# Optimization experiments

Measured on AMD Instinct MI355X. Metric: run time of the kernel, lower is better.

Reference implementation:

```python
import jax, jax.numpy as jnp
import numpy as np

S = 16        # neighbor samples per layer
NL = 2        # number of GNN layers


def setup_inputs() -> dict:
    key = jax.random.key(0)
    ks = jax.random.split(key, 12)
    N_NODES, D, E, NMP, DEG, N_EDGE, B, NC = 50000, 128, 32, 3, 32, 200000, 1024, 8
    sc = 0.05
    return {
        "ids": jax.random.randint(ks[0], (B,), 0, N_NODES, dtype=jnp.int32),
        "feats": jax.random.normal(ks[1], (N_NODES, D), jnp.float32),
        "edge_emb": jax.random.normal(ks[2], (NMP, N_EDGE, E), jnp.float32),
        "adj_nodes": jax.random.randint(ks[3], (NMP, N_NODES, DEG), 0, N_NODES, dtype=jnp.int32),
        "adj_edges": jax.random.randint(ks[4], (NMP, N_NODES, DEG), 0, N_EDGE, dtype=jnp.int32),
        "W_self": jax.random.normal(ks[5], (NMP, NL, D, D), jnp.float32) * sc,
        "W_neigh": jax.random.normal(ks[6], (NMP, NL, D + E, D), jnp.float32) * sc,
        "W_edge": jax.random.normal(ks[7], (NMP, NL, 2 * D + E, E), jnp.float32) * sc,
        "attn": jax.random.normal(ks[8], (D,), jnp.float32) * sc,
        "fc_w": jax.random.normal(ks[9], (D, NC), jnp.float32) * sc,
        "fc_b": jnp.zeros((NC,), jnp.float32),
    }


def reference(ids, feats, edge_emb, adj_nodes, adj_edges, W_self, W_neigh, W_edge, attn, fc_w, fc_b):
    NMP = adj_nodes.shape[0]
    outs = []
    for mp in range(NMP):
        # --- sample neighbor tree (deterministic: first S columns) ---
        cur = ids
        all_feats = [feats[cur]]
        all_edges = []
        for _ in range(NL):
            nb = adj_nodes[mp][cur][:, :S].reshape(-1)     # [N*S]
            eid = adj_edges[mp][cur][:, :S].reshape(-1)    # [N*S]
            all_edges.append(edge_emb[mp][eid])            # [N*S, E]
            cur = nb
            all_feats.append(feats[cur])
        # --- per-layer aggregation + edge update ---
        for l in range(NL):
            new_feats = []
            for k in range(len(all_feats) - 1):
                xs, xn, ee = all_feats[k], all_feats[k + 1], all_edges[k]
                N = xs.shape[0]
                # mean over sampled neighbors of [neigh_feat || edge_emb]
                nin = jnp.concatenate(
                    [xn.reshape(N, S, -1), ee.reshape(N, S, -1)], axis=-1
                ).mean(axis=1)                             # [N, D+E]
                new_feats.append(jax.nn.relu(xs @ W_self[mp, l] + nin @ W_neigh[mp, l]))
            all_feats = new_feats  # dropout is identity in eval mode
            new_edges = []
            for k in range(len(all_edges) - 1):
                xs, xn, ee = all_feats[k], all_feats[k + 1], all_edges[k]
                rep = jnp.repeat(xs, S, axis=0)            # [N*S, D]
                new_edges.append(jax.nn.relu(
                    jnp.concatenate([rep, xn, ee], axis=-1) @ W_edge[mp, l]))
            all_edges = new_edges
        outs.append(all_feats[0])                          # [B, D]
    stacked = jnp.stack(outs)                              # [NMP, B, D]
    # metapath attention fuse
    scores = jnp.tanh(jnp.einsum('mbd,d->mb', stacked, attn))
    beta = jax.nn.softmax(scores, axis=0)
    emb = jnp.einsum('mb,mbd->bd', beta, stacked)          # [B, D]
    # F.normalize(dim=1)
    emb = emb / jnp.maximum(jnp.linalg.norm(emb, axis=1, keepdims=True), 1e-12)
    return emb @ fc_w + fc_b
```

## Files before the change

kernel.cpp:

```cpp
#include <hip/hip_runtime.h>

#define NNODES  50000
#define D       128
#define E       32
#define NMP     3
#define DEG     32
#define NEDGE   200000
#define B       1024
#define NC      8
#define S       16

#define RPM      17408
#define NKT      9
#define WSTRIDE  36864
#define WESTRIDE 9216

#define CONV_TASKS (1600000 + 6 * WSTRIDE + 3 * WESTRIDE)
#define TOT_TASKS  (CONV_TASKS + 3 * RPM)

typedef float f4 __attribute__((ext_vector_type(4)));
typedef short bh8 __attribute__((ext_vector_type(8)));

static __device__ __forceinline__ unsigned short f2bf(float f) {
    unsigned int u = __float_as_uint(f);
    u = u + 0x7FFFu + ((u >> 16) & 1u);
    return (unsigned short)(u >> 16);
}
static __device__ __forceinline__ float bf2f(unsigned short h) {
    return __uint_as_float(((unsigned int)h) << 16);
}

__global__ __launch_bounds__(256) void convsamp_k(
    const float* __restrict__ feats, const float* __restrict__ Ws,
    const float* __restrict__ Wn, const float* __restrict__ We,
    const int* __restrict__ ids, const int* __restrict__ adjn,
    const int* __restrict__ adje,
    unsigned short* __restrict__ fb, unsigned short* __restrict__ WT0,
    unsigned short* __restrict__ WTe, int* __restrict__ gx, int* __restrict__ eid1)
{
    int i = blockIdx.x * 256 + threadIdx.x;
    if (i < 1600000) {
        float4 v = ((const float4*)feats)[i];
        unsigned int p0 = (unsigned int)f2bf(v.x) | ((unsigned int)f2bf(v.y) << 16);
        unsigned int p1 = (unsigned int)f2bf(v.z) | ((unsigned int)f2bf(v.w) << 16);
        ((uint2*)fb)[i] = make_uint2(p0, p1);
    } else if (i < 1600000 + 6 * WSTRIDE) {
        int i2 = i - 1600000;
        int ml = i2 / WSTRIDE, e = i2 % WSTRIDE;
        int j = e & 7, t1 = e >> 3;
        int n = t1 & 127, t2 = t1 >> 7;
        int q = t2 & 3, kt = t2 >> 2;
        int k = kt * 32 + q * 8 + j;
        float v = (k < 128) ? Ws[((size_t)ml * 128 + k) * 128 + n]
                            : Wn[((size_t)ml * 160 + (k - 128)) * 128 + n];
        WT0[(size_t)ml * WSTRIDE + e] = f2bf(v);
    } else if (i < CONV_TASKS) {
        int i3 = i - 1600000 - 6 * WSTRIDE;
        int mp = i3 / WESTRIDE, e = i3 % WESTRIDE;
        int j = e & 7, t1 = e >> 3;
        int n = t1 & 31, t2 = t1 >> 5;
        int q = t2 & 3, kt = t2 >> 2;
        int k = kt * 32 + q * 8 + j;
        float v = We[(((size_t)mp * 2) * 288 + k) * 32 + n];
        WTe[(size_t)mp * WESTRIDE + e] = f2bf(v);
    } else if (i < TOT_TASKS) {
        int i4 = i - CONV_TASKS;
        int mp = i4 / RPM, r = i4 % RPM;
        if (r < 16384) {
            int node = ids[r >> 4];
            gx[mp * RPM + r]   = adjn[((size_t)mp * NNODES + node) * DEG + (r & 15)];
            eid1[mp * 16384 + r] = adje[((size_t)mp * NNODES + node) * DEG + (r & 15)];
        } else {
            gx[mp * RPM + r] = ids[r - 16384];
        }
    }
}

__global__ __launch_bounds__(256) void aggnin_k(
    const unsigned short* __restrict__ fb, const float* __restrict__ edge_emb,
    const int* __restrict__ adjn, const int* __restrict__ adje,
    const int* __restrict__ gx, const int* __restrict__ eid1,
    unsigned short* __restrict__ nin)
{
    const int mp = blockIdx.y;
    const int r = blockIdx.x * 4 + (threadIdx.x >> 6);
    const int t = threadIdx.x & 63;
    const float* ee = edge_emb + (size_t)mp * NEDGE * E;

    const int* ip;
    const int* eix;
    if (r < 16384) {
        int node = __builtin_amdgcn_readfirstlane(gx[mp * RPM + r]);
        ip  = adjn + ((size_t)mp * NNODES + node) * DEG;
        eix = adje + ((size_t)mp * NNODES + node) * DEG;
    } else {
        ip  = gx + mp * RPM + (r - 16384) * S;
        eix = eid1 + mp * 16384 + (r - 16384) * S;
    }

    const int hi = t >> 5, t31 = t & 31;

    unsigned int fv[S];
#pragma unroll
    for (int j = 0; j < S; ++j) {
        int nb = __builtin_amdgcn_readfirstlane(ip[j]);
        fv[j] = ((const unsigned int*)fb)[(size_t)nb * 64 + t];
    }
    float ev[S / 2];
#pragma unroll
    for (int e = 0; e < S / 2; ++e) {
        int e_ev = __builtin_amdgcn_readfirstlane(eix[2 * e]);
        int e_od = __builtin_amdgcn_readfirstlane(eix[2 * e + 1]);
        int edd = hi ? e_od : e_ev;
        ev[e] = ee[(size_t)edd * E + t31];
    }

    float s0 = 0.f, s1 = 0.f, se = 0.f;
#pragma unroll
    for (int j = 0; j < S; ++j) {
        s0 += bf2f((unsigned short)(fv[j] & 0xFFFF));
        s1 += bf2f((unsigned short)(fv[j] >> 16));
    }
#pragma unroll
    for (int e = 0; e < S / 2; ++e) se += ev[e];
    se += __shfl_xor(se, 32);

    const float inv = 1.0f / (float)S;
    unsigned short* row = nin + ((size_t)mp * RPM + r) * 160;
    ((unsigned int*)row)[t] =
        (unsigned int)f2bf(s0 * inv) | ((unsigned int)f2bf(s1 * inv) << 16);
    if (t < E) row[128 + t] = f2bf(se * inv);
}

__global__ __launch_bounds__(256) void gemm_feat_k(
    const unsigned short* __restrict__ fb, const int* __restrict__ gx,
    const unsigned short* __restrict__ nin,
    const unsigned short* __restrict__ WT0,
    unsigned short* __restrict__ outb)
{
    const int mp = blockIdx.y;
    const int w = threadIdx.x >> 6;
    const int l = threadIdx.x & 63;
    const int q = l >> 4, lm = l & 15;
    const int m0 = blockIdx.x * 128 + w * 32;
    const unsigned short* wb = WT0 + (size_t)mp * 2 * WSTRIDE;

    const unsigned short* ap[2];
    const unsigned short* np[2];
#pragma unroll
    for (int mt = 0; mt < 2; ++mt) {
        int row = m0 + mt * 16 + lm;
        int node = gx[mp * RPM + row];
        ap[mt] = fb + (size_t)node * 128;
        np[mt] = nin + ((size_t)mp * RPM + row) * 160;
    }

    f4 acc[2][8];
#pragma unroll
    for (int mt = 0; mt < 2; ++mt)
#pragma unroll
        for (int nt = 0; nt < 8; ++nt) acc[mt][nt] = (f4){0.f, 0.f, 0.f, 0.f};

#pragma unroll
    for (int kt = 0; kt < NKT; ++kt) {
        const int k0 = kt * 32 + q * 8;
        bh8 a[2];
#pragma unroll
        for (int mt = 0; mt < 2; ++mt) {
            const unsigned short* p = (k0 < 128) ? (ap[mt] + k0) : (np[mt] + (k0 - 128));
            a[mt] = *(const bh8*)p;
        }
        const unsigned short* wrow = wb + ((size_t)(kt * 4 + q) * 128 + lm) * 8;
#pragma unroll
        for (int nt = 0; nt < 8; ++nt) {
            bh8 bf = *(const bh8*)(wrow + nt * 16 * 8);
#pragma unroll
            for (int mt = 0; mt < 2; ++mt)
                acc[mt][nt] = __builtin_amdgcn_mfma_f32_16x16x32_bf16(a[mt], bf, acc[mt][nt], 0, 0, 0);
        }
    }

#pragma unroll
    for (int mt = 0; mt < 2; ++mt)
#pragma unroll
        for (int nt = 0; nt < 8; ++nt)
#pragma unroll
            for (int rr = 0; rr < 4; ++rr) {
                int row = m0 + mt * 16 + q * 4 + rr;
                int col = nt * 16 + lm;
                outb[((size_t)mp * RPM + row) * 128 + col] = f2bf(fmaxf(acc[mt][nt][rr], 0.f));
            }
}

__global__ __launch_bounds__(256) void edgeagg_k(
    const unsigned short* __restrict__ fout, const float* __restrict__ edge_emb,
    const int* __restrict__ eid1, const unsigned short* __restrict__ WTe,
    unsigned short* __restrict__ agg1)
{
    const int mp = blockIdx.y;
    const int w = threadIdx.x >> 6, l = threadIdx.x & 63;
    const int q = l >> 4, lm = l & 15;
    const int m0 = blockIdx.x * 128 + w * 32;
    const unsigned short* we = WTe + (size_t)mp * WESTRIDE;
    const unsigned short* f1base = fout + (size_t)mp * RPM * 128;
    const unsigned short* f0base = fout + ((size_t)mp * RPM + 16384) * 128;
    const float* ee = edge_emb + (size_t)mp * NEDGE * E;
    const float inv = 1.0f / (float)S;

    const unsigned short* a1p[2];
    const unsigned short* a0p[2];
    int eidL[2];
#pragma unroll
    for (int mt = 0; mt < 2; ++mt) {
        int row = m0 + mt * 16 + lm;
        a1p[mt] = f1base + (size_t)row * 128;
        a0p[mt] = f0base + (size_t)(row >> 4) * 128;
        eidL[mt] = eid1[mp * 16384 + row];
    }

    f4 acc[2][2];
#pragma unroll
    for (int mt = 0; mt < 2; ++mt) { acc[mt][0] = (f4){0,0,0,0}; acc[mt][1] = (f4){0,0,0,0}; }

#pragma unroll
    for (int kt = 0; kt < NKT; ++kt) {
        const int k0 = kt * 32 + q * 8;
        bh8 a[2];
#pragma unroll
        for (int mt = 0; mt < 2; ++mt) {
            if (kt < 4) {
                a[mt] = *(const bh8*)(a0p[mt] + k0);
            } else if (kt < 8) {
                a[mt] = *(const bh8*)(a1p[mt] + (k0 - 128));
            } else {
                const float* ep = ee + (size_t)eidL[mt] * E + q * 8;
                float4 v0 = *(const float4*)ep;
                float4 v1 = *(const float4*)(ep + 4);
                bh8 tv;
                tv[0] = (short)f2bf(v0.x); tv[1] = (short)f2bf(v0.y);
                tv[2] = (short)f2bf(v0.z); tv[3] = (short)f2bf(v0.w);
                tv[4] = (short)f2bf(v1.x); tv[5] = (short)f2bf(v1.y);
                tv[6] = (short)f2bf(v1.z); tv[7] = (short)f2bf(v1.w);
                a[mt] = tv;
            }
        }
        const unsigned short* wrow = we + ((size_t)(kt * 4 + q) * 32 + lm) * 8;
        bh8 b0 = *(const bh8*)(wrow);
        bh8 b1 = *(const bh8*)(wrow + 16 * 8);
#pragma unroll
        for (int mt = 0; mt < 2; ++mt) {
            acc[mt][0] = __builtin_amdgcn_mfma_f32_16x16x32_bf16(a[mt], b0, acc[mt][0], 0, 0, 0);
            acc[mt][1] = __builtin_amdgcn_mfma_f32_16x16x32_bf16(a[mt], b1, acc[mt][1], 0, 0, 0);
        }
    }

#pragma unroll
    for (int mt = 0; mt < 2; ++mt) {
        int seg = (m0 >> 4) + mt;
#pragma unroll
        for (int nt = 0; nt < 2; ++nt) {
            float ps = 0.f;
#pragma unroll
            for (int rr = 0; rr < 4; ++rr) ps += fmaxf(acc[mt][nt][rr], 0.f);
            ps += __shfl_xor(ps, 16);
            ps += __shfl_xor(ps, 32);
            if (l < 16)
                agg1[((size_t)mp * B + seg) * 160 + 128 + nt * 16 + lm] = f2bf(ps * inv);
        }
    }

#pragma unroll
    for (int mt = 0; mt < 2; ++mt) {
        int seg = (m0 >> 4) + mt;
        const unsigned short* fr = f1base + (size_t)seg * 16 * 128;
        float s0 = 0.f, s1 = 0.f;
#pragma unroll
        for (int j = 0; j < S; ++j) {
            unsigned int u = ((const unsigned int*)(fr + j * 128))[l];
            s0 += bf2f((unsigned short)(u & 0xFFFF));
            s1 += bf2f((unsigned short)(u >> 16));
        }
        ((unsigned int*)(agg1 + ((size_t)mp * B + seg) * 160))[l] =
            (unsigned int)f2bf(s0 * inv) | ((unsigned int)f2bf(s1 * inv) << 16);
    }
}

__global__ __launch_bounds__(256) void feat1fin_k(
    const unsigned short* __restrict__ fout, const unsigned short* __restrict__ agg1,
    const unsigned short* __restrict__ WT0,
    const float* __restrict__ attn, const float* __restrict__ fcw,
    const float* __restrict__ fcb, float* __restrict__ out)
{
    __shared__ float sbuf[NMP][32][132];
    const int w = threadIdx.x >> 6, l = threadIdx.x & 63;
    const int q = l >> 4, lm = l & 15;
    const int m0 = blockIdx.x * 32;

    for (int task = w; task < 6; task += 4) {
        const int mp = task >> 1, mt = task & 1;
        const int row = m0 + mt * 16 + lm;
        const unsigned short* ap = fout + ((size_t)mp * RPM + 16384 + row) * 128;
        const unsigned short* np = agg1 + ((size_t)mp * B + row) * 160;
        const unsigned short* wb = WT0 + ((size_t)mp * 2 + 1) * WSTRIDE;

        f4 acc[8];
#pragma unroll
        for (int nt = 0; nt < 8; ++nt) acc[nt] = (f4){0.f, 0.f, 0.f, 0.f};
#pragma unroll
        for (int kt = 0; kt < NKT; ++kt) {
            const int k0 = kt * 32 + q * 8;
            bh8 a = (k0 < 128) ? *(const bh8*)(ap + k0) : *(const bh8*)(np + (k0 - 128));
            const unsigned short* wrow = wb + ((size_t)(kt * 4 + q) * 128 + lm) * 8;
#pragma unroll
            for (int nt = 0; nt < 8; ++nt) {
                bh8 bf = *(const bh8*)(wrow + nt * 16 * 8);
                acc[nt] = __builtin_amdgcn_mfma_f32_16x16x32_bf16(a, bf, acc[nt], 0, 0, 0);
            }
        }
#pragma unroll
        for (int nt = 0; nt < 8; ++nt)
#pragma unroll
            for (int rr = 0; rr < 4; ++rr)
                sbuf[mp][mt * 16 + q * 4 + rr][nt * 16 + lm] = fmaxf(acc[nt][rr], 0.f);
    }
    __syncthreads();

    const int row = threadIdx.x >> 3;
    const int j = threadIdx.x & 7;
    const int d0 = j * 16;
    float sc[NMP];
#pragma unroll
    for (int mp = 0; mp < NMP; ++mp) {
        float p = 0.f;
#pragma unroll
        for (int d = 0; d < 16; ++d) p += sbuf[mp][row][d0 + d] * attn[d0 + d];
        p += __shfl_xor(p, 1); p += __shfl_xor(p, 2); p += __shfl_xor(p, 4);
        sc[mp] = tanhf(p);
    }
    float mx = fmaxf(sc[0], fmaxf(sc[1], sc[2]));
    float e0 = expf(sc[0] - mx), e1 = expf(sc[1] - mx), e2 = expf(sc[2] - mx);
    float isum = 1.f / (e0 + e1 + e2);
    float b0 = e0 * isum, b1 = e1 * isum, b2 = e2 * isum;

    float emb[16];
    float nn = 0.f;
#pragma unroll
    for (int d = 0; d < 16; ++d) {
        float v = b0 * sbuf[0][row][d0 + d] + b1 * sbuf[1][row][d0 + d]
                + b2 * sbuf[2][row][d0 + d];
        emb[d] = v;
        nn += v * v;
    }
    nn += __shfl_xor(nn, 1); nn += __shfl_xor(nn, 2); nn += __shfl_xor(nn, 4);
    float innorm = 1.f / fmaxf(sqrtf(nn), 1e-12f);
#pragma unroll
    for (int d = 0; d < 16; ++d) emb[d] *= innorm;

#pragma unroll
    for (int c = 0; c < NC; ++c) {
        float p = 0.f;
#pragma unroll
        for (int d = 0; d < 16; ++d) p += emb[d] * fcw[(d0 + d) * NC + c];
        p += __shfl_xor(p, 1); p += __shfl_xor(p, 2); p += __shfl_xor(p, 4);
        if (j == c) out[(size_t)(m0 + row) * NC + c] = p + fcb[c];
    }
}

extern "C" void kernel_launch(void* const* d_in, const int* in_sizes, int n_in,
                              void* d_out, int out_size, void* d_ws, size_t ws_size,
                              hipStream_t stream) {
    const int* ids        = (const int*)d_in[0];
    const float* feats    = (const float*)d_in[1];
    const float* edge_emb = (const float*)d_in[2];
    const int* adjn       = (const int*)d_in[3];
    const int* adje       = (const int*)d_in[4];
    const float* Ws       = (const float*)d_in[5];
    const float* Wn       = (const float*)d_in[6];
    const float* We       = (const float*)d_in[7];
    const float* attn     = (const float*)d_in[8];
    const float* fcw      = (const float*)d_in[9];
    const float* fcb      = (const float*)d_in[10];
    float* out = (float*)d_out;

    char* p = (char*)d_ws;
    unsigned short* WT0 = (unsigned short*)p; p += (size_t)6 * WSTRIDE * 2;
    unsigned short* WTe = (unsigned short*)p; p += (size_t)3 * WESTRIDE * 2;
    unsigned short* fb  = (unsigned short*)p; p += (size_t)NNODES * 128 * 2;
    int* gx   = (int*)p;                      p += (size_t)3 * RPM * 4;
    int* eid1 = (int*)p;                      p += (size_t)3 * 16384 * 4;
    unsigned short* nin  = (unsigned short*)p; p += (size_t)3 * RPM * 160 * 2;
    unsigned short* fout = (unsigned short*)p; p += (size_t)3 * RPM * 128 * 2;
    unsigned short* agg1 = (unsigned short*)p; p += (size_t)3 * B * 160 * 2;

    convsamp_k<<<TOT_TASKS / 256, 256, 0, stream>>>(feats, Ws, Wn, We, ids, adjn, adje,
                                                    fb, WT0, WTe, gx, eid1);
    aggnin_k<<<dim3(RPM / 4, 3), 256, 0, stream>>>(fb, edge_emb, adjn, adje, gx, eid1, nin);
    gemm_feat_k<<<dim3(136, 3), 256, 0, stream>>>(fb, gx, nin, WT0, fout);
    edgeagg_k<<<dim3(128, 3), 256, 0, stream>>>(fout, edge_emb, eid1, WTe, agg1);
    feat1fin_k<<<32, 256, 0, stream>>>(fout, agg1, WT0, attn, fcw, fcb, out);
}
```

Before: 253.1 us.

## Fuse neighbor aggregation into feature GEMM via shared-memory staging

Merges the mean-aggregation kernel and the feature GEMM into one kernel: each block gathers 32 rows of self and aggregated neighbor features into LDS, then the four waves each compute a 32-column slice with MFMA. This removes the global round-trip of the nin intermediate and one kernel launch. In exchange, the gather phase now processes 8 rows sequentially per wave, and each wave reloads the A tile from LDS, which may reduce memory-level parallelism in the latency-bound gather.

```diff
diff --git a/kernel.cpp b/kernel.cpp
--- a/kernel.cpp
+++ b/kernel.cpp
@@ -68,7 +68,7 @@
         int mp = i4 / RPM, r = i4 % RPM;
         if (r < 16384) {
             int node = ids[r >> 4];
-            gx[mp * RPM + r]   = adjn[((size_t)mp * NNODES + node) * DEG + (r & 15)];
+            gx[mp * RPM + r]     = adjn[((size_t)mp * NNODES + node) * DEG + (r & 15)];
             eid1[mp * 16384 + r] = adje[((size_t)mp * NNODES + node) * DEG + (r & 15)];
         } else {
             gx[mp * RPM + r] = ids[r - 16384];
@@ -76,90 +76,73 @@
     }
 }
 
-__global__ __launch_bounds__(256) void aggnin_k(
+__global__ __launch_bounds__(256) void aggfeat_k(
     const unsigned short* __restrict__ fb, const float* __restrict__ edge_emb,
     const int* __restrict__ adjn, const int* __restrict__ adje,
     const int* __restrict__ gx, const int* __restrict__ eid1,
-    unsigned short* __restrict__ nin)
+    const unsigned short* __restrict__ WT0,
+    unsigned short* __restrict__ fout)
 {
+    __shared__ unsigned short Asm[32][136];
+    __shared__ unsigned short Nsm[32][168];
     const int mp = blockIdx.y;
-    const int r = blockIdx.x * 4 + (threadIdx.x >> 6);
-    const int t = threadIdx.x & 63;
+    const int w = threadIdx.x >> 6, t = threadIdx.x & 63;
+    const int r0 = blockIdx.x * 32;
     const float* ee = edge_emb + (size_t)mp * NEDGE * E;
-
-    const int* ip;
-    const int* eix;
-    if (r < 16384) {
-        int node = __builtin_amdgcn_readfirstlane(gx[mp * RPM + r]);
-        ip  = adjn + ((size_t)mp * NNODES + node) * DEG;
-        eix = adje + ((size_t)mp * NNODES + node) * DEG;
-    } else {
-        ip  = gx + mp * RPM + (r - 16384) * S;
-        eix = eid1 + mp * 16384 + (r - 16384) * S;
-    }
-
     const int hi = t >> 5, t31 = t & 31;
-
-    unsigned int fv[S];
-#pragma unroll
-    for (int j = 0; j < S; ++j) {
-        int nb = __builtin_amdgcn_readfirstlane(ip[j]);
-        fv[j] = ((const unsigned int*)fb)[(size_t)nb * 64 + t];
-    }
-    float ev[S / 2];
-#pragma unroll
-    for (int e = 0; e < S / 2; ++e) {
-        int e_ev = __builtin_amdgcn_readfirstlane(eix[2 * e]);
-        int e_od = __builtin_amdgcn_readfirstlane(eix[2 * e + 1]);
-        int edd = hi ? e_od : e_ev;
-        ev[e] = ee[(size_t)edd * E + t31];
-    }
-
-    float s0 = 0.f, s1 = 0.f, se = 0.f;
-#pragma unroll
-    for (int j = 0; j < S; ++j) {
-        s0 += bf2f((unsigned short)(fv[j] & 0xFFFF));
-        s1 += bf2f((unsigned short)(fv[j] >> 16));
-    }
-#pragma unroll
-    for (int e = 0; e < S / 2; ++e) se += ev[e];
-    se += __shfl_xor(se, 32);
-
     const float inv = 1.0f / (float)S;
-    unsigned short* row = nin + ((size_t)mp * RPM + r) * 160;
-    ((unsigned int*)row)[t] =
-        (unsigned int)f2bf(s0 * inv) | ((unsigned int)f2bf(s1 * inv) << 16);
-    if (t < E) row[128 + t] = f2bf(se * inv);
-}
-
-__global__ __launch_bounds__(256) void gemm_feat_k(
-    const unsigned short* __restrict__ fb, const int* __restrict__ gx,
-    const unsigned short* __restrict__ nin,
-    const unsigned short* __restrict__ WT0,
-    unsigned short* __restrict__ outb)
-{
-    const int mp = blockIdx.y;
-    const int w = threadIdx.x >> 6;
-    const int l = threadIdx.x & 63;
-    const int q = l >> 4, lm = l & 15;
-    const int m0 = blockIdx.x * 128 + w * 32;
+
+    for (int rr = 0; rr < 8; ++rr) {
+        const int lr = w * 8 + rr;
+        const int r = r0 + lr;
+        const int self = __builtin_amdgcn_readfirstlane(gx[mp * RPM + r]);
+        const int* ip;
+        const int* eix;
+        if (r < 16384) {
+            ip  = adjn + ((size_t)mp * NNODES + self) * DEG;
+            eix = adje + ((size_t)mp * NNODES + self) * DEG;
+        } else {
+            ip  = gx + mp * RPM + (r - 16384) * S;
+            eix = eid1 + mp * 16384 + (r - 16384) * S;
+        }
+        unsigned int av = ((const unsigned int*)fb)[(size_t)self * 64 + t];
+        unsigned int fv[S];
+#pragma unroll
+        for (int j = 0; j < S; ++j) {
+            int nb = __builtin_amdgcn_readfirstlane(ip[j]);
+            fv[j] = ((const unsigned int*)fb)[(size_t)nb * 64 + t];
+        }
+        float ev[S / 2];
+#pragma unroll
+        for (int e = 0; e < S / 2; ++e) {
+            int e_ev = __builtin_amdgcn_readfirstlane(eix[2 * e]);
+            int e_od = __builtin_amdgcn_readfirstlane(eix[2 * e + 1]);
+            int edd = hi ? e_od : e_ev;
+            ev[e] = ee[(size_t)edd * E + t31];
+        }
+        float s0 = 0.f, s1 = 0.f, se = 0.f;
+#pragma unroll
+        for (int j = 0; j < S; ++j) {
+            s0 += bf2f((unsigned short)(fv[j] & 0xFFFF));
+            s1 += bf2f((unsigned short)(fv[j] >> 16));
+        }
+#pragma unroll
+        for (int e = 0; e < S / 2; ++e) se += ev[e];
+        se += __shfl_xor(se, 32);
+
+        ((unsigned int*)&Asm[lr][0])[t] = av;
+        ((unsigned int*)&Nsm[lr][0])[t] =
+            (unsigned int)f2bf(s0 * inv) | ((unsigned int)f2bf(s1 * inv) << 16);
+        if (t < E) Nsm[lr][128 + t] = f2bf(se * inv);
+    }
+    __syncthreads();
+
+    const int q = t >> 4, lm = t & 15;
     const unsigned short* wb = WT0 + (size_t)mp * 2 * WSTRIDE;
 
-    const unsigned short* ap[2];
-    const unsigned short* np[2];
-#pragma unroll
-    for (int mt = 0; mt < 2; ++mt) {
-        int row = m0 + mt * 16 + lm;
-        int node = gx[mp * RPM + row];
-        ap[mt] = fb + (size_t)node * 128;
-        np[mt] = nin + ((size_t)mp * RPM + row) * 160;
-    }
-
-    f4 acc[2][8];
-#pragma unroll
-    for (int mt = 0; mt < 2; ++mt)
-#pragma unroll
-        for (int nt = 0; nt < 8; ++nt) acc[mt][nt] = (f4){0.f, 0.f, 0.f, 0.f};
+    f4 acc[2][2];
+#pragma unroll
+    for (int mt = 0; mt < 2; ++mt) { acc[mt][0] = (f4){0,0,0,0}; acc[mt][1] = (f4){0,0,0,0}; }
 
 #pragma unroll
     for (int kt = 0; kt < NKT; ++kt) {
@@ -167,28 +150,29 @@
         bh8 a[2];
 #pragma unroll
         for (int mt = 0; mt < 2; ++mt) {
-            const unsigned short* p = (k0 < 128) ? (ap[mt] + k0) : (np[mt] + (k0 - 128));
-            a[mt] = *(const bh8*)p;
+            int lr = mt * 16 + lm;
+            a[mt] = (k0 < 128) ? *(const bh8*)&Asm[lr][k0]
+                               : *(const bh8*)&Nsm[lr][k0 - 128];
         }
         const unsigned short* wrow = wb + ((size_t)(kt * 4 + q) * 128 + lm) * 8;
 #pragma unroll
-        for (int nt = 0; nt < 8; ++nt) {
-            bh8 bf = *(const bh8*)(wrow + nt * 16 * 8);
+        for (int ntl = 0; ntl < 2; ++ntl) {
+            bh8 bf = *(const bh8*)(wrow + (w * 2 + ntl) * 16 * 8);
 #pragma unroll
             for (int mt = 0; mt < 2; ++mt)
-                acc[mt][nt] = __builtin_amdgcn_mfma_f32_16x16x32_bf16(a[mt], bf, acc[mt][nt], 0, 0, 0);
+                acc[mt][ntl] = __builtin_amdgcn_mfma_f32_16x16x32_bf16(a[mt], bf, acc[mt][ntl], 0, 0, 0);
         }
     }
 
 #pragma unroll
     for (int mt = 0; mt < 2; ++mt)
 #pragma unroll
-        for (int nt = 0; nt < 8; ++nt)
+        for (int ntl = 0; ntl < 2; ++ntl)
 #pragma unroll
             for (int rr = 0; rr < 4; ++rr) {
-                int row = m0 + mt * 16 + q * 4 + rr;
-                int col = nt * 16 + lm;
-                outb[((size_t)mp * RPM + row) * 128 + col] = f2bf(fmaxf(acc[mt][nt][rr], 0.f));
+                int row = r0 + mt * 16 + q * 4 + rr;
+                int col = (w * 2 + ntl) * 16 + lm;
+                fout[((size_t)mp * RPM + row) * 128 + col] = f2bf(fmaxf(acc[mt][ntl][rr], 0.f));
             }
 }
 
@@ -388,14 +372,13 @@
     unsigned short* fb  = (unsigned short*)p; p += (size_t)NNODES * 128 * 2;
     int* gx   = (int*)p;                      p += (size_t)3 * RPM * 4;
     int* eid1 = (int*)p;                      p += (size_t)3 * 16384 * 4;
-    unsigned short* nin  = (unsigned short*)p; p += (size_t)3 * RPM * 160 * 2;
     unsigned short* fout = (unsigned short*)p; p += (size_t)3 * RPM * 128 * 2;
     unsigned short* agg1 = (unsigned short*)p; p += (size_t)3 * B * 160 * 2;
 
     convsamp_k<<<TOT_TASKS / 256, 256, 0, stream>>>(feats, Ws, Wn, We, ids, adjn, adje,
                                                     fb, WT0, WTe, gx, eid1);
-    aggnin_k<<<dim3(RPM / 4, 3), 256, 0, stream>>>(fb, edge_emb, adjn, adje, gx, eid1, nin);
-    gemm_feat_k<<<dim3(136, 3), 256, 0, stream>>>(fb, gx, nin, WT0, fout);
+    aggfeat_k<<<dim3(RPM / 32, 3), 256, 0, stream>>>(fb, edge_emb, adjn, adje, gx, eid1,
+                                                     WT0, fout);
     edgeagg_k<<<dim3(128, 3), 256, 0, stream>>>(fout, edge_emb, eid1, WTe, agg1);
     feat1fin_k<<<32, 256, 0, stream>>>(fout, agg1, WT0, attn, fcw, fcb, out);
 }
```

Result: faster. 242.9 us (-4.0%).
